# Kernel tuning notes

Measured on AMD Instinct MI355X. Metric: run time of the kernel, lower is better.

## Reference

```python
import jax, jax.numpy as jnp
import numpy as np

B, N, VF, EF, DV, DE, LN = 64, 64, 32, 16, 128, 128, 4
EPS_INNER = 128.0  # BatchNorm1d(MAX_N, internal_d_vert): 2nd positional arg is eps (faithful to source bug)
EPS_BN = 1e-5


def gev_layer(v_in, e_in, evW, evb, eW, eb, vW, vb, relu=True):
    act = jax.nn.relu if relu else (lambda x: x)
    ev = v_in @ evW + evb                                   # [B,N,De]
    # outer_v_sum: ev.unsqueeze(1) + ev.unsqueeze(2) -> [B,N,N,De]
    e_out = act(e_in @ eW + eb + ev[:, None, :, :] + ev[:, :, None, :])
    per_v_e = e_out.sum(axis=1)                             # sum-aggregate over dim 1
    v_out = act(jnp.concatenate([per_v_e, v_in], axis=-1) @ vW + vb)
    return v_out, e_out


def bn_flat(v, g, b):
    # BatchNorm1d(N*VF) on [B, N*VF] in training mode (biased var)
    x = v.reshape(-1, N * VF)
    mu = x.mean(axis=0)
    var = x.var(axis=0)
    x = (x - mu) * jax.lax.rsqrt(var + EPS_BN) * g + b
    return x.reshape(-1, N, VF)


def bn_inner(v, g, b):
    # BatchNorm1d(MAX_N, eps=128) on [B, N, D]: channels are the N axis, stats over (B, D)
    mu = v.mean(axis=(0, 2), keepdims=True)
    var = v.var(axis=(0, 2), keepdims=True)
    return (v - mu) * jax.lax.rsqrt(var + EPS_INNER) * g[None, :, None] + b[None, :, None]


def setup_inputs() -> dict:
    key = jax.random.key(0)
    ks = jax.random.split(key, 24)
    s = 0.01  # force_lin_init with init_noise=0.01, biases zero
    nrm = lambda k, shp: jax.random.normal(k, shp, dtype=jnp.float32) * s
    inp = {
        "v": jax.random.normal(ks[0], (B, N, VF), dtype=jnp.float32),
        "e": jax.random.normal(ks[1], (B, N, N, EF), dtype=jnp.float32),
        "bn_in_g": jnp.ones((N * VF,), jnp.float32),
        "bn_in_b": jnp.zeros((N * VF,), jnp.float32),
        "g1_evW": nrm(ks[2], (VF, DE)), "g1_evb": jnp.zeros((DE,), jnp.float32),
        "g1_eW": nrm(ks[3], (EF, DE)), "g1_eb": jnp.zeros((DE,), jnp.float32),
        "g1_vW": nrm(ks[4], (VF + DE, DV)), "g1_vb": jnp.zeros((DV,), jnp.float32),
        "inn_evW": nrm(ks[5], (LN, DV, DE)), "inn_evb": jnp.zeros((LN, DE), jnp.float32),
        "inn_eW": nrm(ks[6], (LN, DE, DE)), "inn_eb": jnp.zeros((LN, DE), jnp.float32),
        "inn_vW": nrm(ks[7], (LN, DV + DE, DV)), "inn_vb": jnp.zeros((LN, DV), jnp.float32),
        "bn_g": jnp.ones((LN, N), jnp.float32),
        "bn_b": jnp.zeros((LN, N), jnp.float32),
        "g3_evW": nrm(ks[8], (DV, 1)), "g3_evb": jnp.zeros((1,), jnp.float32),
        "g3_eW": nrm(ks[9], (DE, 1)), "g3_eb": jnp.zeros((1,), jnp.float32),
        "g3_vW": nrm(ks[10], (DV + 1, 1)), "g3_vb": jnp.zeros((1,), jnp.float32),
    }
    return inp


def reference(v, e, bn_in_g, bn_in_b, g1_evW, g1_evb, g1_eW, g1_eb, g1_vW, g1_vb,
              inn_evW, inn_evb, inn_eW, inn_eb, inn_vW, inn_vb, bn_g, bn_b,
              g3_evW, g3_evb, g3_eW, g3_eb, g3_vW, g3_vb):
    v = bn_flat(v, bn_in_g, bn_in_b)
    v, e = gev_layer(v, e, g1_evW, g1_evb, g1_eW, g1_eb, g1_vW, g1_vb)
    for i in range(LN):
        v_next, e_next = gev_layer(v, e, inn_evW[i], inn_evb[i], inn_eW[i], inn_eb[i], inn_vW[i], inn_vb[i])
        v = v_next + v  # resnet
        e = e_next + e
        v = bn_inner(v, bn_g[i], bn_b[i])
    v, e = gev_layer(v, e, g3_evW, g3_evb, g3_eW, g3_eb, g3_vW, g3_vb, relu=False)
    return v, e
```

## Files before the change

### kernel.cpp

```cpp
#include <hip/hip_runtime.h>
#include <hip/hip_bf16.h>


typedef __bf16 bf16_t;
typedef __bf16 bf16x8 __attribute__((ext_vector_type(8)));
typedef __bf16 bf16x4 __attribute__((ext_vector_type(4)));
typedef float f32x4 __attribute__((ext_vector_type(4)));

__global__ __launch_bounds__(256) void k_bn_in(const float* __restrict__ vin,
    const float* __restrict__ g, const float* __restrict__ bt,
    float* __restrict__ v0) {
  int ch = blockIdx.x * 256 + threadIdx.x;
  float s = 0.f, s2 = 0.f;
  for (int b = 0; b < 64; ++b) { float x = vin[b * 2048 + ch]; s += x; s2 += x * x; }
  float mu = s * (1.f / 64.f);
  float var = s2 * (1.f / 64.f) - mu * mu;
  float sc = rsqrtf(var + 1e-5f) * g[ch];
  float bb = bt[ch];
  for (int b = 0; b < 64; ++b) {
    float x = vin[b * 2048 + ch];
    v0[b * 2048 + ch] = (x - mu) * sc + bb;
  }
}

__global__ __launch_bounds__(256) void k_prep_wt(const float* __restrict__ eW,
    bf16_t* __restrict__ Wt) {
  int idx = blockIdx.x * 256 + threadIdx.x;
  int l = idx >> 14, r = idx & 16383, n = r >> 7, k = r & 127;
  Wt[idx] = (bf16_t)eW[(l << 14) + (k << 7) + n];
}

template <int K>
__global__ __launch_bounds__(128) void k_ev(const float* __restrict__ v_in,
    const float* __restrict__ W, const float* __restrict__ bias,
    float* __restrict__ out) {
  __shared__ float rows[8][K];
  const int r0 = blockIdx.x * 8;
  const int c = threadIdx.x;
  for (int idx = c; idx < 8 * K; idx += 128) {
    int rr = idx / K, kk = idx % K;
    rows[rr][kk] = v_in[(r0 + rr) * K + kk];
  }
  __syncthreads();
  float acc[8];
  const float bv = bias[c];
#pragma unroll
  for (int r = 0; r < 8; ++r) acc[r] = bv;
  for (int k4 = 0; k4 < K; k4 += 4) {
    float w0 = W[(k4 + 0) * 128 + c], w1 = W[(k4 + 1) * 128 + c];
    float w2 = W[(k4 + 2) * 128 + c], w3 = W[(k4 + 3) * 128 + c];
#pragma unroll
    for (int r = 0; r < 8; ++r) {
      float4 x = *(const float4*)&rows[r][k4];
      acc[r] += x.x * w0 + x.y * w1 + x.z * w2 + x.w * w3;
    }
  }
#pragma unroll
  for (int r = 0; r < 8; ++r) out[(r0 + r) * 128 + c] = acc[r];
}

__global__ __launch_bounds__(128) void k_evbn(float* __restrict__ v,
    const float* __restrict__ stats, const float* __restrict__ g,
    const float* __restrict__ bt, const float* __restrict__ W,
    const float* __restrict__ bias, float* __restrict__ out) {
  __shared__ float rows[8][128];
  const int r0 = blockIdx.x * 8;
  const int c = threadIdx.x;
#pragma unroll
  for (int rr = 0; rr < 8; ++rr) {
    int n = (r0 + rr) & 63;
    float mu = stats[n] * (1.f / 8192.f);
    float var = stats[64 + n] * (1.f / 8192.f) - mu * mu;
    float sc = rsqrtf(var + 128.f) * g[n];
    float x = (v[(r0 + rr) * 128 + c] - mu) * sc + bt[n];
    rows[rr][c] = x;
    v[(r0 + rr) * 128 + c] = x;
  }
  __syncthreads();
  float acc[8];
  const float bv = bias[c];
#pragma unroll
  for (int r = 0; r < 8; ++r) acc[r] = bv;
  for (int k4 = 0; k4 < 128; k4 += 4) {
    float w0 = W[(k4 + 0) * 128 + c], w1 = W[(k4 + 1) * 128 + c];
    float w2 = W[(k4 + 2) * 128 + c], w3 = W[(k4 + 3) * 128 + c];
#pragma unroll
    for (int r = 0; r < 8; ++r) {
      float4 x = *(const float4*)&rows[r][k4];
      acc[r] += x.x * w0 + x.y * w1 + x.z * w2 + x.w * w3;
    }
  }
#pragma unroll
  for (int r = 0; r < 8; ++r) out[(r0 + r) * 128 + c] = acc[r];
}

__global__ __launch_bounds__(256) void k_edge_g1(const float* __restrict__ e0,
    const float* __restrict__ eW, const float* __restrict__ eb,
    const float* __restrict__ ev, bf16_t* __restrict__ e_ws,
    float* __restrict__ pve) {
  __shared__ bf16_t A0s[2][64][40];
  __shared__ bf16_t Os[2][64][136];
  const int b = blockIdx.x >> 5, j0 = (blockIdx.x & 31) * 2;
  const int tid = threadIdx.x;
  const int lane = tid & 63, w = tid >> 6;
  const int quad = lane >> 4, l16 = lane & 15;
#pragma unroll
  for (int t = 0; t < 2; ++t) {
    int idx = tid + t * 256;
    int row = idx >> 3, off = (idx & 7) * 4;
    int jc = off >> 4, k = off & 15;
    f32x4 x = *(const f32x4*)&e0[((b * 64 + row) * 64 + j0) * 16 + off];
    bf16x4 y;
#pragma unroll
    for (int r = 0; r < 4; ++r) y[r] = (bf16_t)x[r];
    *(bf16x4*)&A0s[jc][row][k] = y;
    bf16x4 z = {(bf16_t)0.f, (bf16_t)0.f, (bf16_t)0.f, (bf16_t)0.f};
    *(bf16x4*)&A0s[jc][row][16 + k] = z;
  }
  const int c0[2] = {w * 32 + quad * 4, w * 32 + 16 + quad * 4};
  bf16x8 wf[2];
#pragma unroll
  for (int nt = 0; nt < 2; ++nt) {
    const int c = w * 32 + nt * 16 + l16;
#pragma unroll
    for (int jj = 0; jj < 8; ++jj)
      wf[nt][jj] = (quad < 2) ? (bf16_t)eW[(quad * 8 + jj) * 128 + c] : (bf16_t)0.f;
  }
  f32x4 acc[2][4][2];
  {
    f32x4 ebv[2], evj[2][2], evi[4][2];
#pragma unroll
    for (int nt = 0; nt < 2; ++nt) {
      ebv[nt] = *(const f32x4*)&eb[c0[nt]];
#pragma unroll
      for (int jc = 0; jc < 2; ++jc)
        evj[jc][nt] = *(const f32x4*)&ev[(b * 64 + j0 + jc) * 128 + c0[nt]];
#pragma unroll
      for (int mt = 0; mt < 4; ++mt)
        evi[mt][nt] = *(const f32x4*)&ev[(b * 64 + mt * 16 + l16) * 128 + c0[nt]];
    }
#pragma unroll
    for (int jc = 0; jc < 2; ++jc)
#pragma unroll
      for (int mt = 0; mt < 4; ++mt)
#pragma unroll
        for (int nt = 0; nt < 2; ++nt)
          acc[jc][mt][nt] = ebv[nt] + evj[jc][nt] + evi[mt][nt];
  }
  __syncthreads();
#pragma unroll
  for (int jc = 0; jc < 2; ++jc) {
#pragma unroll
    for (int mt = 0; mt < 4; ++mt) {
      bf16x8 ef = *(const bf16x8*)&A0s[jc][mt * 16 + l16][quad * 8];
#pragma unroll
      for (int nt = 0; nt < 2; ++nt)
        acc[jc][mt][nt] = __builtin_amdgcn_mfma_f32_16x16x32_bf16(wf[nt], ef, acc[jc][mt][nt], 0, 0, 0);
    }
  }
#pragma unroll
  for (int jc = 0; jc < 2; ++jc) {
#pragma unroll
    for (int nt = 0; nt < 2; ++nt) {
      f32x4 ps = {0.f, 0.f, 0.f, 0.f};
#pragma unroll
      for (int mt = 0; mt < 4; ++mt) {
        const int i = mt * 16 + l16;
        bf16x4 outv;
#pragma unroll
        for (int r = 0; r < 4; ++r) {
          float vv = fmaxf(acc[jc][mt][nt][r], 0.f);
          ps[r] += vv;
          outv[r] = (bf16_t)vv;
        }
        *(bf16x4*)&Os[jc][i][c0[nt]] = outv;
      }
#pragma unroll
      for (int m = 1; m <= 8; m <<= 1) {
#pragma unroll
        for (int r = 0; r < 4; ++r) ps[r] += __shfl_xor(ps[r], m);
      }
      if (l16 == 0) *(f32x4*)&pve[(b * 64 + j0 + jc) * 128 + c0[nt]] = ps;
    }
  }
  __syncthreads();
#pragma unroll
  for (int t = 0; t < 8; ++t) {
    int idx = tid + t * 256;
    int row = idx >> 5, off = (idx & 31) * 8;
    int jc = off >> 7, c = off & 127;
    *(int4*)&e_ws[((b * 64 + row) * 64 + j0) * 128 + off] = *(const int4*)&Os[jc][row][c];
  }
}

__global__ __launch_bounds__(128) void k_v_g1(const float* __restrict__ pve,
    const float* __restrict__ v0, const float* __restrict__ vW,
    const float* __restrict__ vb, float* __restrict__ v) {
  __shared__ float in[8][160];
  const int r0 = blockIdx.x * 8;
  const int c = threadIdx.x;
#pragma unroll
  for (int t = 0; t < 8; ++t) {
    int idx = c + t * 128;
    int rr = idx >> 7, k = idx & 127;
    in[rr][k] = pve[(r0 + rr) * 128 + k];
  }
#pragma unroll
  for (int t = 0; t < 2; ++t) {
    int idx = c + t * 128;
    int rr = idx >> 5, k = idx & 31;
    in[rr][128 + k] = v0[(r0 + rr) * 32 + k];
  }
  __syncthreads();
  float acc[8];
  const float bv = vb[c];
#pragma unroll
  for (int r = 0; r < 8; ++r) acc[r] = bv;
  for (int k4 = 0; k4 < 160; k4 += 4) {
    float w0 = vW[(k4 + 0) * 128 + c], w1 = vW[(k4 + 1) * 128 + c];
    float w2 = vW[(k4 + 2) * 128 + c], w3 = vW[(k4 + 3) * 128 + c];
#pragma unroll
    for (int r = 0; r < 8; ++r) {
      float4 x = *(const float4*)&in[r][k4];
      acc[r] += x.x * w0 + x.y * w1 + x.z * w2 + x.w * w3;
    }
  }
#pragma unroll
  for (int r = 0; r < 8; ++r) v[(r0 + r) * 128 + c] = fmaxf(acc[r], 0.f);
}

__global__ __launch_bounds__(256) void k_edge_inner(bf16_t* __restrict__ e_ws,
    const bf16_t* __restrict__ Wt, const float* __restrict__ eb,
    const float* __restrict__ ev, float* __restrict__ pve) {
  __shared__ bf16_t As[2][64][136];
  const int b = blockIdx.x >> 5, j0 = (blockIdx.x & 31) * 2;
  const int tid = threadIdx.x;
  const int lane = tid & 63, w = tid >> 6;
  const int quad = lane >> 4, l16 = lane & 15;
  int4 stg[8];
#pragma unroll
  for (int t = 0; t < 8; ++t) {
    int idx = tid + t * 256;
    int row = idx >> 5, off = (idx & 31) * 8;
    stg[t] = *(const int4*)&e_ws[((b * 64 + row) * 64 + j0) * 128 + off];
  }
  bf16x8 wf[2][4];
#pragma unroll
  for (int nt = 0; nt < 2; ++nt)
#pragma unroll
    for (int ks = 0; ks < 4; ++ks)
      wf[nt][ks] = *(const bf16x8*)&Wt[(w * 32 + nt * 16 + l16) * 128 + ks * 32 + quad * 8];
  const int c0[2] = {w * 32 + quad * 4, w * 32 + 16 + quad * 4};
  f32x4 acc[2][4][2];
  {
    f32x4 ebv[2], evj[2][2], evi[4][2];
#pragma unroll
    for (int nt = 0; nt < 2; ++nt) {
      ebv[nt] = *(const f32x4*)&eb[c0[nt]];
#pragma unroll
      for (int jc = 0; jc < 2; ++jc)
        evj[jc][nt] = *(const f32x4*)&ev[(b * 64 + j0 + jc) * 128 + c0[nt]];
#pragma unroll
      for (int mt = 0; mt < 4; ++mt)
        evi[mt][nt] = *(const f32x4*)&ev[(b * 64 + mt * 16 + l16) * 128 + c0[nt]];
    }
#pragma unroll
    for (int jc = 0; jc < 2; ++jc)
#pragma unroll
      for (int mt = 0; mt < 4; ++mt)
#pragma unroll
        for (int nt = 0; nt < 2; ++nt)
          acc[jc][mt][nt] = ebv[nt] + evj[jc][nt] + evi[mt][nt];
  }
#pragma unroll
  for (int t = 0; t < 8; ++t) {
    int idx = tid + t * 256;
    int row = idx >> 5, off = (idx & 31) * 8;
    *(int4*)&As[off >> 7][row][off & 127] = stg[t];
  }
  __syncthreads();
#pragma unroll
  for (int ks = 0; ks < 4; ++ks) {
    bf16x8 ef[2][4];
#pragma unroll
    for (int jc = 0; jc < 2; ++jc)
#pragma unroll
      for (int mt = 0; mt < 4; ++mt)
        ef[jc][mt] = *(const bf16x8*)&As[jc][mt * 16 + l16][ks * 32 + quad * 8];
#pragma unroll
    for (int jc = 0; jc < 2; ++jc)
#pragma unroll
      for (int mt = 0; mt < 4; ++mt)
#pragma unroll
        for (int nt = 0; nt < 2; ++nt)
          acc[jc][mt][nt] = __builtin_amdgcn_mfma_f32_16x16x32_bf16(wf[nt][ks], ef[jc][mt], acc[jc][mt][nt], 0, 0, 0);
  }
  __syncthreads();
#pragma unroll
  for (int jc = 0; jc < 2; ++jc) {
#pragma unroll
    for (int nt = 0; nt < 2; ++nt) {
      f32x4 ps = {0.f, 0.f, 0.f, 0.f};
#pragma unroll
      for (int mt = 0; mt < 4; ++mt) {
        const int i = mt * 16 + l16;
        bf16x4 eo = *(const bf16x4*)&As[jc][i][c0[nt]];
        bf16x4 outv;
#pragma unroll
        for (int r = 0; r < 4; ++r) {
          float vv = fmaxf(acc[jc][mt][nt][r], 0.f);
          ps[r] += vv;
          outv[r] = (bf16_t)(vv + (float)eo[r]);
        }
        *(bf16x4*)&As[jc][i][c0[nt]] = outv;
      }
#pragma unroll
      for (int m = 1; m <= 8; m <<= 1) {
#pragma unroll
        for (int r = 0; r < 4; ++r) ps[r] += __shfl_xor(ps[r], m);
      }
      if (l16 == 0) *(f32x4*)&pve[(b * 64 + j0 + jc) * 128 + c0[nt]] = ps;
    }
  }
  __syncthreads();
#pragma unroll
  for (int t = 0; t < 8; ++t) {
    int idx = tid + t * 256;
    int row = idx >> 5, off = (idx & 31) * 8;
    *(int4*)&e_ws[((b * 64 + row) * 64 + j0) * 128 + off] = *(const int4*)&As[off >> 7][row][off & 127];
  }
}

__global__ __launch_bounds__(128) void k_v_inner(const float* __restrict__ pve,
    float* __restrict__ v, const float* __restrict__ vW,
    const float* __restrict__ vb, float* __restrict__ stats) {
  __shared__ float in[8][256];
  __shared__ float outs[8][132];
  const int r0 = blockIdx.x * 8;
  const int c = threadIdx.x;
#pragma unroll
  for (int t = 0; t < 8; ++t) {
    int idx = c + t * 128;
    int rr = idx >> 7, k = idx & 127;
    in[rr][k] = pve[(r0 + rr) * 128 + k];
    in[rr][128 + k] = v[(r0 + rr) * 128 + k];
  }
  __syncthreads();
  float acc[8];
  const float bv = vb[c];
#pragma unroll
  for (int r = 0; r < 8; ++r) acc[r] = bv;
  for (int k4 = 0; k4 < 256; k4 += 4) {
    float w0 = vW[(k4 + 0) * 128 + c], w1 = vW[(k4 + 1) * 128 + c];
    float w2 = vW[(k4 + 2) * 128 + c], w3 = vW[(k4 + 3) * 128 + c];
#pragma unroll
    for (int r = 0; r < 8; ++r) {
      float4 x = *(const float4*)&in[r][k4];
      acc[r] += x.x * w0 + x.y * w1 + x.z * w2 + x.w * w3;
    }
  }
#pragma unroll
  for (int r = 0; r < 8; ++r) {
    float val = fmaxf(acc[r], 0.f) + in[r][128 + c];
    outs[r][c] = val;
    v[(r0 + r) * 128 + c] = val;
  }
  __syncthreads();
  if (c < 8) {
    float s = 0.f, s2 = 0.f;
    for (int k = 0; k < 128; ++k) { float x = outs[c][k]; s += x; s2 += x * x; }
    int n = (r0 + c) & 63;
    atomicAdd(&stats[n], s);
    atomicAdd(&stats[64 + n], s2);
  }
}

__global__ __launch_bounds__(256) void k_bn_apply(float* __restrict__ v,
    const float* __restrict__ stats, const float* __restrict__ g,
    const float* __restrict__ bt) {
  int idx = blockIdx.x * 256 + threadIdx.x;
  int n = (idx >> 7) & 63;
  float mu = stats[n] * (1.f / 8192.f);
  float var = stats[64 + n] * (1.f / 8192.f) - mu * mu;
  float sc = rsqrtf(var + 128.f) * g[n];
  v[idx] = (v[idx] - mu) * sc + bt[n];
}

__global__ __launch_bounds__(256) void k_ev3(const float* __restrict__ v,
    const float* __restrict__ W, const float* __restrict__ bias,
    float* __restrict__ ev3) {
  int r = blockIdx.x * 4 + (threadIdx.x >> 6);
  int lane = threadIdx.x & 63;
  float acc = v[r * 128 + lane] * W[lane] + v[r * 128 + 64 + lane] * W[64 + lane];
#pragma unroll
  for (int m = 1; m < 64; m <<= 1) acc += __shfl_xor(acc, m);
  if (lane == 0) ev3[r] = acc + bias[0];
}

__global__ __launch_bounds__(256) void k_edge_g3(const bf16_t* __restrict__ e_ws,
    const float* __restrict__ eW3, const float* __restrict__ eb3,
    const float* __restrict__ ev3, float* __restrict__ out_e,
    float* __restrict__ pve3) {
  __shared__ float W3[128];
  const int b = blockIdx.x >> 6, i = blockIdx.x & 63;
  const int tid = threadIdx.x;
  if (tid < 128) W3[tid] = eW3[tid];
  __syncthreads();
  const int j = tid >> 2, cs = (tid & 3) * 32;
  const bf16_t* ep = &e_ws[(size_t)((b * 64 + i) * 64 + j) * 128 + cs];
  float acc = 0.f;
#pragma unroll
  for (int t = 0; t < 4; ++t) {
    bf16x8 x = *(const bf16x8*)&ep[t * 8];
#pragma unroll
    for (int u = 0; u < 8; ++u) acc += (float)x[u] * W3[cs + t * 8 + u];
  }
  acc += __shfl_xor(acc, 1);
  acc += __shfl_xor(acc, 2);
  if ((tid & 3) == 0) {
    float s = acc + eb3[0] + ev3[b * 64 + i] + ev3[b * 64 + j];
    out_e[(b * 64 + i) * 64 + j] = s;
    atomicAdd(&pve3[b * 64 + j], s);
  }
}

__global__ __launch_bounds__(256) void k_v_g3(const float* __restrict__ v,
    const float* __restrict__ pve3, const float* __restrict__ vW,
    const float* __restrict__ vb, float* __restrict__ out_v) {
  int r = blockIdx.x * 4 + (threadIdx.x >> 6);
  int lane = threadIdx.x & 63;
  float acc = v[r * 128 + lane] * vW[1 + lane] + v[r * 128 + 64 + lane] * vW[65 + lane];
#pragma unroll
  for (int m = 1; m < 64; m <<= 1) acc += __shfl_xor(acc, m);
  if (lane == 0) out_v[r] = acc + pve3[r] * vW[0] + vb[0];
}

extern "C" void kernel_launch(void* const* d_in, const int* in_sizes, int n_in,
                              void* d_out, int out_size, void* d_ws, size_t ws_size,
                              hipStream_t stream) {
  const float* in_v    = (const float*)d_in[0];
  const float* in_e    = (const float*)d_in[1];
  const float* bn_in_g = (const float*)d_in[2];
  const float* bn_in_b = (const float*)d_in[3];
  const float* g1_evW  = (const float*)d_in[4];
  const float* g1_evb  = (const float*)d_in[5];
  const float* g1_eW   = (const float*)d_in[6];
  const float* g1_eb   = (const float*)d_in[7];
  const float* g1_vW   = (const float*)d_in[8];
  const float* g1_vb   = (const float*)d_in[9];
  const float* inn_evW = (const float*)d_in[10];
  const float* inn_evb = (const float*)d_in[11];
  const float* inn_eW  = (const float*)d_in[12];
  const float* inn_eb  = (const float*)d_in[13];
  const float* inn_vW  = (const float*)d_in[14];
  const float* inn_vb  = (const float*)d_in[15];
  const float* bn_g    = (const float*)d_in[16];
  const float* bn_b    = (const float*)d_in[17];
  const float* g3_evW  = (const float*)d_in[18];
  const float* g3_evb  = (const float*)d_in[19];
  const float* g3_eW   = (const float*)d_in[20];
  const float* g3_eb   = (const float*)d_in[21];
  const float* g3_vW   = (const float*)d_in[22];
  const float* g3_vb   = (const float*)d_in[23];

  char* ws = (char*)d_ws;
  bf16_t* e_ws = (bf16_t*)(ws);
  float* v     = (float*)(ws + 67108864);
  float* ev    = (float*)(ws + 69206016);
  float* pve   = (float*)(ws + 71303168);
  float* v0    = (float*)(ws + 73400320);
  bf16_t* Wt   = (bf16_t*)(ws + 73924608);
  float* ev3   = (float*)(ws + 74055680);
  float* pve3  = (float*)(ws + 74072064);
  float* stats = (float*)(ws + 74088448);

  float* out_v = (float*)d_out;
  float* out_e = (float*)d_out + 4096;

  hipMemsetAsync(pve3, 0, 16384 + 2048, stream);
  k_bn_in<<<8, 256, 0, stream>>>(in_v, bn_in_g, bn_in_b, v0);
  k_prep_wt<<<256, 256, 0, stream>>>(inn_eW, Wt);

  k_ev<32><<<512, 128, 0, stream>>>(v0, g1_evW, g1_evb, ev);
  k_edge_g1<<<2048, 256, 0, stream>>>(in_e, g1_eW, g1_eb, ev, e_ws, pve);
  k_v_g1<<<512, 128, 0, stream>>>(pve, v0, g1_vW, g1_vb, v);

  for (int l = 0; l < 4; ++l) {
    if (l == 0)
      k_ev<128><<<512, 128, 0, stream>>>(v, inn_evW, inn_evb, ev);
    else
      k_evbn<<<512, 128, 0, stream>>>(v, stats + (l - 1) * 128, bn_g + (l - 1) * 64,
                                      bn_b + (l - 1) * 64, inn_evW + l * 16384,
                                      inn_evb + l * 128, ev);
    k_edge_inner<<<2048, 256, 0, stream>>>(e_ws, Wt + l * 16384, inn_eb + l * 128, ev, pve);
    k_v_inner<<<512, 128, 0, stream>>>(pve, v, inn_vW + l * 32768, inn_vb + l * 128,
                                       stats + l * 128);
  }
  k_bn_apply<<<2048, 256, 0, stream>>>(v, stats + 3 * 128, bn_g + 192, bn_b + 192);

  k_ev3<<<1024, 256, 0, stream>>>(v, g3_evW, g3_evb, ev3);
  k_edge_g3<<<4096, 256, 0, stream>>>(e_ws, g3_eW, g3_eb, ev3, out_e, pve3);
  k_v_g3<<<1024, 256, 0, stream>>>(v, pve3, g3_vW, g3_vb, out_v);
}
```

Before: 422.0 us.

## Fuse vertex updates into edge kernels and BN apply into final layer

Each edge kernel now computes the vertex MLP for the two rows it owns, using an in-shared-memory edge-sum. This removes the separate k_v_g1/k_v_inner launches and the pve round trip through global memory. The final BatchNorm apply and ev3 projection move into k_edge_g3/k_v_g3, and the input BN, weight transpose and zeroing are merged into one prep kernel that replaces the memset. In exchange, every block rereads the full vertex weight matrix for only two rows, and every g3 block redundantly normalizes 64 vertex rows. That adds L2 traffic and tail work to the edge kernels.

```diff
diff --git a/kernel.cpp b/kernel.cpp
--- a/kernel.cpp
+++ b/kernel.cpp
@@ -7,27 +7,31 @@
 typedef __bf16 bf16x4 __attribute__((ext_vector_type(4)));
 typedef float f32x4 __attribute__((ext_vector_type(4)));
 
-__global__ __launch_bounds__(256) void k_bn_in(const float* __restrict__ vin,
+__global__ __launch_bounds__(256) void k_prep(const float* __restrict__ vin,
     const float* __restrict__ g, const float* __restrict__ bt,
-    float* __restrict__ v0) {
-  int ch = blockIdx.x * 256 + threadIdx.x;
-  float s = 0.f, s2 = 0.f;
-  for (int b = 0; b < 64; ++b) { float x = vin[b * 2048 + ch]; s += x; s2 += x * x; }
-  float mu = s * (1.f / 64.f);
-  float var = s2 * (1.f / 64.f) - mu * mu;
-  float sc = rsqrtf(var + 1e-5f) * g[ch];
-  float bb = bt[ch];
-  for (int b = 0; b < 64; ++b) {
-    float x = vin[b * 2048 + ch];
-    v0[b * 2048 + ch] = (x - mu) * sc + bb;
-  }
-}
-
-__global__ __launch_bounds__(256) void k_prep_wt(const float* __restrict__ eW,
-    bf16_t* __restrict__ Wt) {
-  int idx = blockIdx.x * 256 + threadIdx.x;
-  int l = idx >> 14, r = idx & 16383, n = r >> 7, k = r & 127;
-  Wt[idx] = (bf16_t)eW[(l << 14) + (k << 7) + n];
+    const float* __restrict__ eW, float* __restrict__ v0,
+    bf16_t* __restrict__ Wt, float* __restrict__ pve3, float* __restrict__ stats) {
+  const int blk = blockIdx.x, tid = threadIdx.x;
+  if (blk < 8) {
+    int ch = blk * 256 + tid;
+    float s = 0.f, s2 = 0.f;
+    for (int b = 0; b < 64; ++b) { float x = vin[b * 2048 + ch]; s += x; s2 += x * x; }
+    float mu = s * (1.f / 64.f);
+    float var = s2 * (1.f / 64.f) - mu * mu;
+    float sc = rsqrtf(var + 1e-5f) * g[ch];
+    float bb = bt[ch];
+    for (int b = 0; b < 64; ++b) {
+      float x = vin[b * 2048 + ch];
+      v0[b * 2048 + ch] = (x - mu) * sc + bb;
+    }
+  } else if (blk < 264) {
+    int idx = (blk - 8) * 256 + tid;
+    int l = idx >> 14, r = idx & 16383, n = r >> 7, k = r & 127;
+    Wt[idx] = (bf16_t)eW[(l << 14) + (k << 7) + n];
+  } else {
+    for (int i = tid; i < 4096; i += 256) pve3[i] = 0.f;
+    for (int i = tid; i < 512; i += 256) stats[i] = 0.f;
+  }
 }
 
 template <int K>
@@ -96,10 +100,13 @@
 
 __global__ __launch_bounds__(256) void k_edge_g1(const float* __restrict__ e0,
     const float* __restrict__ eW, const float* __restrict__ eb,
-    const float* __restrict__ ev, bf16_t* __restrict__ e_ws,
-    float* __restrict__ pve) {
+    const float* __restrict__ ev, const float* __restrict__ v0,
+    const float* __restrict__ vW, const float* __restrict__ vb,
+    bf16_t* __restrict__ e_ws, float* __restrict__ v) {
   __shared__ bf16_t A0s[2][64][40];
   __shared__ bf16_t Os[2][64][136];
+  __shared__ float vr0[2][32];
+  __shared__ float pves[2][128];
   const int b = blockIdx.x >> 5, j0 = (blockIdx.x & 31) * 2;
   const int tid = threadIdx.x;
   const int lane = tid & 63, w = tid >> 6;
@@ -117,6 +124,7 @@
     bf16x4 z = {(bf16_t)0.f, (bf16_t)0.f, (bf16_t)0.f, (bf16_t)0.f};
     *(bf16x4*)&A0s[jc][row][16 + k] = z;
   }
+  if (tid < 64) vr0[tid >> 5][tid & 31] = v0[(b * 64 + j0 + (tid >> 5)) * 32 + (tid & 31)];
   const int c0[2] = {w * 32 + quad * 4, w * 32 + 16 + quad * 4};
   bf16x8 wf[2];
 #pragma unroll
@@ -180,7 +188,7 @@
 #pragma unroll
         for (int r = 0; r < 4; ++r) ps[r] += __shfl_xor(ps[r], m);
       }
-      if (l16 == 0) *(f32x4*)&pve[(b * 64 + j0 + jc) * 128 + c0[nt]] = ps;
+      if (l16 == 0) *(f32x4*)&pves[jc][c0[nt]] = ps;
     }
   }
   __syncthreads();
@@ -191,48 +199,24 @@
     int jc = off >> 7, c = off & 127;
     *(int4*)&e_ws[((b * 64 + row) * 64 + j0) * 128 + off] = *(const int4*)&Os[jc][row][c];
   }
-}
-
-__global__ __launch_bounds__(128) void k_v_g1(const float* __restrict__ pve,
-    const float* __restrict__ v0, const float* __restrict__ vW,
-    const float* __restrict__ vb, float* __restrict__ v) {
-  __shared__ float in[8][160];
-  const int r0 = blockIdx.x * 8;
-  const int c = threadIdx.x;
-#pragma unroll
-  for (int t = 0; t < 8; ++t) {
-    int idx = c + t * 128;
-    int rr = idx >> 7, k = idx & 127;
-    in[rr][k] = pve[(r0 + rr) * 128 + k];
-  }
-#pragma unroll
-  for (int t = 0; t < 2; ++t) {
-    int idx = c + t * 128;
-    int rr = idx >> 5, k = idx & 31;
-    in[rr][128 + k] = v0[(r0 + rr) * 32 + k];
-  }
-  __syncthreads();
-  float acc[8];
-  const float bv = vb[c];
-#pragma unroll
-  for (int r = 0; r < 8; ++r) acc[r] = bv;
-  for (int k4 = 0; k4 < 160; k4 += 4) {
-    float w0 = vW[(k4 + 0) * 128 + c], w1 = vW[(k4 + 1) * 128 + c];
-    float w2 = vW[(k4 + 2) * 128 + c], w3 = vW[(k4 + 3) * 128 + c];
-#pragma unroll
-    for (int r = 0; r < 8; ++r) {
-      float4 x = *(const float4*)&in[r][k4];
-      acc[r] += x.x * w0 + x.y * w1 + x.z * w2 + x.w * w3;
-    }
-  }
-#pragma unroll
-  for (int r = 0; r < 8; ++r) v[(r0 + r) * 128 + c] = fmaxf(acc[r], 0.f);
+  {
+    const int jc = tid >> 7, c = tid & 127;
+    float a = vb[c];
+    for (int k = 0; k < 128; ++k) a += pves[jc][k] * vW[k * 128 + c];
+#pragma unroll
+    for (int k = 0; k < 32; ++k) a += vr0[jc][k] * vW[(128 + k) * 128 + c];
+    v[(b * 64 + j0 + jc) * 128 + c] = fmaxf(a, 0.f);
+  }
 }
 
 __global__ __launch_bounds__(256) void k_edge_inner(bf16_t* __restrict__ e_ws,
     const bf16_t* __restrict__ Wt, const float* __restrict__ eb,
-    const float* __restrict__ ev, float* __restrict__ pve) {
+    const float* __restrict__ ev, float* __restrict__ v,
+    const float* __restrict__ vW, const float* __restrict__ vb,
+    float* __restrict__ stats) {
   __shared__ bf16_t As[2][64][136];
+  __shared__ float vrow[2][128];
+  __shared__ float pves[2][128];
   const int b = blockIdx.x >> 5, j0 = (blockIdx.x & 31) * 2;
   const int tid = threadIdx.x;
   const int lane = tid & 63, w = tid >> 6;
@@ -244,6 +228,7 @@
     int row = idx >> 5, off = (idx & 31) * 8;
     stg[t] = *(const int4*)&e_ws[((b * 64 + row) * 64 + j0) * 128 + off];
   }
+  if (tid < 256) vrow[tid >> 7][tid & 127] = v[(b * 64 + j0 + (tid >> 7)) * 128 + (tid & 127)];
   bf16x8 wf[2][4];
 #pragma unroll
   for (int nt = 0; nt < 2; ++nt)
@@ -319,7 +304,7 @@
 #pragma unroll
         for (int r = 0; r < 4; ++r) ps[r] += __shfl_xor(ps[r], m);
       }
-      if (l16 == 0) *(f32x4*)&pve[(b * 64 + j0 + jc) * 128 + c0[nt]] = ps;
+      if (l16 == 0) *(f32x4*)&pves[jc][c0[nt]] = ps;
     }
   }
   __syncthreads();
@@ -329,107 +314,102 @@
     int row = idx >> 5, off = (idx & 31) * 8;
     *(int4*)&e_ws[((b * 64 + row) * 64 + j0) * 128 + off] = *(const int4*)&As[off >> 7][row][off & 127];
   }
-}
-
-__global__ __launch_bounds__(128) void k_v_inner(const float* __restrict__ pve,
-    float* __restrict__ v, const float* __restrict__ vW,
-    const float* __restrict__ vb, float* __restrict__ stats) {
-  __shared__ float in[8][256];
-  __shared__ float outs[8][132];
-  const int r0 = blockIdx.x * 8;
-  const int c = threadIdx.x;
+  {
+    const int jc = tid >> 7, c = tid & 127;
+    float a = vb[c];
+    for (int k = 0; k < 128; ++k) a += pves[jc][k] * vW[k * 128 + c];
+    for (int k = 0; k < 128; ++k) a += vrow[jc][k] * vW[(128 + k) * 128 + c];
+    float val = fmaxf(a, 0.f) + vrow[jc][c];
+    v[(b * 64 + j0 + jc) * 128 + c] = val;
+    float s = val, s2 = val * val;
+#pragma unroll
+    for (int m = 1; m < 64; m <<= 1) {
+      s += __shfl_xor(s, m);
+      s2 += __shfl_xor(s2, m);
+    }
+    if (lane == 0) {
+      atomicAdd(&stats[j0 + jc], s);
+      atomicAdd(&stats[64 + j0 + jc], s2);
+    }
+  }
+}
+
+__global__ __launch_bounds__(256) void k_edge_g3(const bf16_t* __restrict__ e_ws,
+    const float* __restrict__ vv, const float* __restrict__ stats3,
+    const float* __restrict__ g, const float* __restrict__ bt,
+    const float* __restrict__ evW3, const float* __restrict__ evb3,
+    const float* __restrict__ eW3, const float* __restrict__ eb3,
+    float* __restrict__ out_e, float* __restrict__ pve3) {
+  __shared__ float vbn[64][132];
+  __shared__ float scs[64], shs[64];
+  __shared__ float W3e[128], W3ee[128];
+  __shared__ float ev3s[64];
+  const int b = blockIdx.x >> 6, i = blockIdx.x & 63;
+  const int tid = threadIdx.x;
+  if (tid < 64) {
+    float mu = stats3[tid] * (1.f / 8192.f);
+    float var = stats3[64 + tid] * (1.f / 8192.f) - mu * mu;
+    float sc = rsqrtf(var + 128.f) * g[tid];
+    scs[tid] = sc;
+    shs[tid] = bt[tid] - mu * sc;
+  }
+  if (tid < 128) W3ee[tid] = eW3[tid];
+  else W3e[tid - 128] = evW3[tid - 128];
+  __syncthreads();
 #pragma unroll
   for (int t = 0; t < 8; ++t) {
-    int idx = c + t * 128;
-    int rr = idx >> 7, k = idx & 127;
-    in[rr][k] = pve[(r0 + rr) * 128 + k];
-    in[rr][128 + k] = v[(r0 + rr) * 128 + k];
-  }
-  __syncthreads();
-  float acc[8];
-  const float bv = vb[c];
-#pragma unroll
-  for (int r = 0; r < 8; ++r) acc[r] = bv;
-  for (int k4 = 0; k4 < 256; k4 += 4) {
-    float w0 = vW[(k4 + 0) * 128 + c], w1 = vW[(k4 + 1) * 128 + c];
-    float w2 = vW[(k4 + 2) * 128 + c], w3 = vW[(k4 + 3) * 128 + c];
-#pragma unroll
-    for (int r = 0; r < 8; ++r) {
-      float4 x = *(const float4*)&in[r][k4];
-      acc[r] += x.x * w0 + x.y * w1 + x.z * w2 + x.w * w3;
-    }
-  }
-#pragma unroll
-  for (int r = 0; r < 8; ++r) {
-    float val = fmaxf(acc[r], 0.f) + in[r][128 + c];
-    outs[r][c] = val;
-    v[(r0 + r) * 128 + c] = val;
-  }
-  __syncthreads();
-  if (c < 8) {
-    float s = 0.f, s2 = 0.f;
-    for (int k = 0; k < 128; ++k) { float x = outs[c][k]; s += x; s2 += x * x; }
-    int n = (r0 + c) & 63;
-    atomicAdd(&stats[n], s);
-    atomicAdd(&stats[64 + n], s2);
-  }
-}
-
-__global__ __launch_bounds__(256) void k_bn_apply(float* __restrict__ v,
-    const float* __restrict__ stats, const float* __restrict__ g,
-    const float* __restrict__ bt) {
-  int idx = blockIdx.x * 256 + threadIdx.x;
-  int n = (idx >> 7) & 63;
-  float mu = stats[n] * (1.f / 8192.f);
-  float var = stats[64 + n] * (1.f / 8192.f) - mu * mu;
-  float sc = rsqrtf(var + 128.f) * g[n];
-  v[idx] = (v[idx] - mu) * sc + bt[n];
-}
-
-__global__ __launch_bounds__(256) void k_ev3(const float* __restrict__ v,
-    const float* __restrict__ W, const float* __restrict__ bias,
-    float* __restrict__ ev3) {
+    int idx = t * 1024 + tid * 4;
+    int row = idx >> 7, c = idx & 127;
+    f32x4 x = *(const f32x4*)&vv[(b * 64 + row) * 128 + c];
+    f32x4 y = x * scs[row] + shs[row];
+    *(f32x4*)&vbn[row][c] = y;
+  }
+  __syncthreads();
+  {
+    int r = tid >> 2, q = tid & 3;
+    float a = 0.f;
+#pragma unroll
+    for (int u = 0; u < 32; ++u) a += vbn[r][q * 32 + u] * W3e[q * 32 + u];
+    a += __shfl_xor(a, 1);
+    a += __shfl_xor(a, 2);
+    if (q == 0) ev3s[r] = a + evb3[0];
+  }
+  __syncthreads();
+  {
+    const int j = tid >> 2, cs = (tid & 3) * 32;
+    const bf16_t* ep = &e_ws[(size_t)((b * 64 + i) * 64 + j) * 128 + cs];
+    float acc = 0.f;
+#pragma unroll
+    for (int t = 0; t < 4; ++t) {
+      bf16x8 x = *(const bf16x8*)&ep[t * 8];
+#pragma unroll
+      for (int u = 0; u < 8; ++u) acc += (float)x[u] * W3ee[cs + t * 8 + u];
+    }
+    acc += __shfl_xor(acc, 1);
+    acc += __shfl_xor(acc, 2);
+    if ((tid & 3) == 0) {
+      float s = acc + eb3[0] + ev3s[i] + ev3s[j];
+      out_e[(b * 64 + i) * 64 + j] = s;
+      atomicAdd(&pve3[b * 64 + j], s);
+    }
+  }
+}
+
+__global__ __launch_bounds__(256) void k_v_g3(const float* __restrict__ vv,
+    const float* __restrict__ stats3, const float* __restrict__ g,
+    const float* __restrict__ bt, const float* __restrict__ pve3,
+    const float* __restrict__ vW, const float* __restrict__ vb,
+    float* __restrict__ out_v) {
   int r = blockIdx.x * 4 + (threadIdx.x >> 6);
   int lane = threadIdx.x & 63;
-  float acc = v[r * 128 + lane] * W[lane] + v[r * 128 + 64 + lane] * W[64 + lane];
-#pragma unroll
-  for (int m = 1; m < 64; m <<= 1) acc += __shfl_xor(acc, m);
-  if (lane == 0) ev3[r] = acc + bias[0];
-}
-
-__global__ __launch_bounds__(256) void k_edge_g3(const bf16_t* __restrict__ e_ws,
-    const float* __restrict__ eW3, const float* __restrict__ eb3,
-    const float* __restrict__ ev3, float* __restrict__ out_e,
-    float* __restrict__ pve3) {
-  __shared__ float W3[128];
-  const int b = blockIdx.x >> 6, i = blockIdx.x & 63;
-  const int tid = threadIdx.x;
-  if (tid < 128) W3[tid] = eW3[tid];
-  __syncthreads();
-  const int j = tid >> 2, cs = (tid & 3) * 32;
-  const bf16_t* ep = &e_ws[(size_t)((b * 64 + i) * 64 + j) * 128 + cs];
-  float acc = 0.f;
-#pragma unroll
-  for (int t = 0; t < 4; ++t) {
-    bf16x8 x = *(const bf16x8*)&ep[t * 8];
-#pragma unroll
-    for (int u = 0; u < 8; ++u) acc += (float)x[u] * W3[cs + t * 8 + u];
-  }
-  acc += __shfl_xor(acc, 1);
-  acc += __shfl_xor(acc, 2);
-  if ((tid & 3) == 0) {
-    float s = acc + eb3[0] + ev3[b * 64 + i] + ev3[b * 64 + j];
-    out_e[(b * 64 + i) * 64 + j] = s;
-    atomicAdd(&pve3[b * 64 + j], s);
-  }
-}
-
-__global__ __launch_bounds__(256) void k_v_g3(const float* __restrict__ v,
-    const float* __restrict__ pve3, const float* __restrict__ vW,
-    const float* __restrict__ vb, float* __restrict__ out_v) {
-  int r = blockIdx.x * 4 + (threadIdx.x >> 6);
-  int lane = threadIdx.x & 63;
-  float acc = v[r * 128 + lane] * vW[1 + lane] + v[r * 128 + 64 + lane] * vW[65 + lane];
+  int n = r & 63;
+  float mu = stats3[n] * (1.f / 8192.f);
+  float var = stats3[64 + n] * (1.f / 8192.f) - mu * mu;
+  float sc = rsqrtf(var + 128.f) * g[n];
+  float sh = bt[n] - mu * sc;
+  float x1 = vv[r * 128 + lane] * sc + sh;
+  float x2 = vv[r * 128 + 64 + lane] * sc + sh;
+  float acc = x1 * vW[1 + lane] + x2 * vW[65 + lane];
 #pragma unroll
   for (int m = 1; m < 64; m <<= 1) acc += __shfl_xor(acc, m);
   if (lane == 0) out_v[r] = acc + pve3[r] * vW[0] + vb[0];
@@ -467,23 +447,18 @@
   bf16_t* e_ws = (bf16_t*)(ws);
   float* v     = (float*)(ws + 67108864);
   float* ev    = (float*)(ws + 69206016);
-  float* pve   = (float*)(ws + 71303168);
   float* v0    = (float*)(ws + 73400320);
   bf16_t* Wt   = (bf16_t*)(ws + 73924608);
-  float* ev3   = (float*)(ws + 74055680);
   float* pve3  = (float*)(ws + 74072064);
   float* stats = (float*)(ws + 74088448);
 
   float* out_v = (float*)d_out;
   float* out_e = (float*)d_out + 4096;
 
-  hipMemsetAsync(pve3, 0, 16384 + 2048, stream);
-  k_bn_in<<<8, 256, 0, stream>>>(in_v, bn_in_g, bn_in_b, v0);
-  k_prep_wt<<<256, 256, 0, stream>>>(inn_eW, Wt);
+  k_prep<<<265, 256, 0, stream>>>(in_v, bn_in_g, bn_in_b, inn_eW, v0, Wt, pve3, stats);
 
   k_ev<32><<<512, 128, 0, stream>>>(v0, g1_evW, g1_evb, ev);
-  k_edge_g1<<<2048, 256, 0, stream>>>(in_e, g1_eW, g1_eb, ev, e_ws, pve);
-  k_v_g1<<<512, 128, 0, stream>>>(pve, v0, g1_vW, g1_vb, v);
+  k_edge_g1<<<2048, 256, 0, stream>>>(in_e, g1_eW, g1_eb, ev, v0, g1_vW, g1_vb, e_ws, v);
 
   for (int l = 0; l < 4; ++l) {
     if (l == 0)
@@ -492,13 +467,13 @@
       k_evbn<<<512, 128, 0, stream>>>(v, stats + (l - 1) * 128, bn_g + (l - 1) * 64,
                                       bn_b + (l - 1) * 64, inn_evW + l * 16384,
                                       inn_evb + l * 128, ev);
-    k_edge_inner<<<2048, 256, 0, stream>>>(e_ws, Wt + l * 16384, inn_eb + l * 128, ev, pve);
-    k_v_inner<<<512, 128, 0, stream>>>(pve, v, inn_vW + l * 32768, inn_vb + l * 128,
-                                       stats + l * 128);
-  }
-  k_bn_apply<<<2048, 256, 0, stream>>>(v, stats + 3 * 128, bn_g + 192, bn_b + 192);
-
-  k_ev3<<<1024, 256, 0, stream>>>(v, g3_evW, g3_evb, ev3);
-  k_edge_g3<<<4096, 256, 0, stream>>>(e_ws, g3_eW, g3_eb, ev3, out_e, pve3);
-  k_v_g3<<<1024, 256, 0, stream>>>(v, pve3, g3_vW, g3_vb, out_v);
-}
+    k_edge_inner<<<2048, 256, 0, stream>>>(e_ws, Wt + l * 16384, inn_eb + l * 128, ev,
+                                           v, inn_vW + l * 32768, inn_vb + l * 128,
+                                           stats + l * 128);
+  }
+
+  k_edge_g3<<<4096, 256, 0, stream>>>(e_ws, v, stats + 384, bn_g + 192, bn_b + 192,
+                                      g3_evW, g3_evb, g3_eW, g3_eb, out_e, pve3);
+  k_v_g3<<<1024, 256, 0, stream>>>(v, stats + 384, bn_g + 192, bn_b + 192, pve3,
+                                   g3_vW, g3_vb, out_v);
+}
```

After: 532.0 us. +26.1%, slower.
